# Kernel tuning notes

Hardware: AMD Instinct MI355X
Metric: run time of the kernel (lower is better)

Reference implementation:

```python
import jax, jax.numpy as jnp
import numpy as np

WS = (4, 4, 4)          # window size (s, h, w)
NUM_HEADS = 6
DIM = 192               # kv channels C
CS = 2                  # channel_scale; q/out channels = DIM // CS
B = 256                 # num_windows * batch


def _rel_pos_index(ws):
    """Reproduces the module's relative_position_index buffer (shape [8shw, 2shw])."""
    s, h, w = ws
    cs = np.repeat(np.arange(s), 2)
    ch = np.repeat(np.arange(h), 2)
    cw = np.repeat(np.arange(w), 2)
    coords = np.stack(np.meshgrid(cs, ch, cw, indexing='ij'))   # (3, 2s, 2h, 2w)
    cf = coords.reshape(3, -1)                                   # (3, T), T = 8shw
    rel = cf[:, :, None] - cf[:, None, :]                        # (3, T, T)
    rel = rel[:, :, ::4]                                         # (3, T, T//4)
    rel = np.ascontiguousarray(rel.transpose(1, 2, 0))           # (T, T//4, 3)
    rel[:, :, 0] += s - 1
    rel[:, :, 1] += h - 1
    rel[:, :, 2] += w - 1
    rel[:, :, 0] *= 3 * h - 1
    rel[:, :, 1] *= 2 * h - 1
    return rel.sum(-1).astype(np.int32)                          # (T, T//4)


def setup_inputs() -> dict:
    key = jax.random.key(0)
    ks = jax.random.split(key, 9)
    s, h, w = WS
    qN = 8 * s * h * w          # 512 query tokens per window
    N = qN // 4                 # 128 key/value tokens per window
    C = DIM
    qC = DIM // CS
    table_len = (4 * s - 1) * (4 * h - 1) * (4 * w - 1)
    return {
        'kv': jax.random.normal(ks[0], (B, N, C), jnp.float32),
        'q': jax.random.normal(ks[1], (B, qN, qC), jnp.float32),
        'w_kv': jax.random.normal(ks[2], (C, 2 * C), jnp.float32) * 0.02,
        'b_kv': jnp.zeros((2 * C,), jnp.float32),
        'w_q': jax.random.normal(ks[3], (qC, C), jnp.float32) * 0.02,
        'b_q': jnp.zeros((C,), jnp.float32),
        'w_proj': jax.random.normal(ks[4], (C, qC), jnp.float32) * 0.02,
        'b_proj': jnp.zeros((qC,), jnp.float32),
        'bias_table': jax.random.normal(ks[5], (table_len, NUM_HEADS), jnp.float32) * 0.02,
        'rel_index': jnp.asarray(_rel_pos_index(WS)),
    }


def reference(kv, q, w_kv, b_kv, w_q, b_q, w_proj, b_proj, bias_table, rel_index):
    B_, N, C = kv.shape
    d = C // NUM_HEADS
    scale = d ** -0.5
    # project kv -> k, v : (B_, nH, N, d)
    kvp = (kv @ w_kv + b_kv).reshape(B_, N, 2, NUM_HEADS, d)
    k = kvp[:, :, 0].transpose(0, 2, 1, 3)
    v = kvp[:, :, 1].transpose(0, 2, 1, 3)
    # project q : (B_, nH, qN, d), pre-scaled
    qp = (q @ w_q + b_q).reshape(B_, -1, NUM_HEADS, d).transpose(0, 2, 1, 3) * scale
    attn = jnp.einsum('bhqd,bhkd->bhqk', qp, k)          # (B_, nH, qN, N)
    bias = bias_table[rel_index]                          # (qN, N, nH) gather
    attn = attn + bias.transpose(2, 0, 1)[None]           # + (1, nH, qN, N)
    attn = jax.nn.softmax(attn, axis=-1)
    out = jnp.einsum('bhqk,bhkd->bhqd', attn, v)          # (B_, nH, qN, d)
    out = out.transpose(0, 2, 1, 3).reshape(B_, -1, C)    # (B_, qN, C)
    return out @ w_proj + b_proj                          # (B_, qN, C//CS)
```

## Files before the change

### kernel.cpp

```cpp
#include <hip/hip_runtime.h>
#include <hip/hip_bf16.h>

#define B_    256
#define NKV   128
#define NQ    512
#define CDIM  192
#define QCDIM 96
#define NH    6
#define DH    32
#define SCALE 0.17677669529663687f
#define LOG2E 1.4426950408889634f

typedef __hip_bfloat16 bf16;
typedef __attribute__((ext_vector_type(8))) short s16x8;
typedef __attribute__((ext_vector_type(4))) short s16x4;
typedef __attribute__((ext_vector_type(4))) float f32x4;
#define MFMA16(a, b, c) __builtin_amdgcn_mfma_f32_16x16x32_bf16(a, b, c, 0, 0, 0)

__device__ __forceinline__ float b2f(short s) {
    return __uint_as_float(((unsigned)(unsigned short)s) << 16);
}

#define OFF_BIASF 0
#define OFF_WKVF  786432
#define OFF_WQF   933888
#define OFF_WPF   970752
#define OFF_KF    1007616
#define OFF_VF    13590528

__global__ __launch_bounds__(256)
void precomp_all(const float* __restrict__ w_kv, const float* __restrict__ w_q,
                 const float* __restrict__ w_proj, const float* __restrict__ bias_table,
                 const int* __restrict__ rel_index,
                 bf16* __restrict__ biasF, bf16* __restrict__ wkvF,
                 bf16* __restrict__ wqF, bf16* __restrict__ wpF)
{
    const int i = blockIdx.x * 256 + threadIdx.x;
    if (i < 98304) {
        const int lane = i & 63, tl = (i >> 6) & 7, rowblk = (i >> 9) & 31, h = i >> 14;
        const int quad = lane >> 4, l16 = lane & 15;
        const int kvi = tl * 16 + l16;
        __align__(8) bf16 vr[4];
        #pragma unroll
        for (int r = 0; r < 4; ++r) {
            const int qrow = rowblk * 16 + quad * 4 + r;
            vr[r] = __float2bfloat16(bias_table[rel_index[qrow * NKV + kvi] * NH + h] * LOG2E);
        }
        *(uint2*)&biasF[i * 4] = *(uint2*)vr;
    } else if (i < 98304 + 73728) {
        const int i1 = i - 98304;
        const int j = i1 & 7, lane = (i1 >> 3) & 63, kk = (i1 >> 9) % 6, nt = i1 / 3072;
        const int quad = lane >> 4, l16 = lane & 15;
        wkvF[i1] = __float2bfloat16(w_kv[(kk * 32 + quad * 8 + j) * (2 * CDIM) + nt * 16 + l16]);
    } else if (i < 98304 + 92160) {
        const int i2 = i - 98304 - 73728;
        const int j = i2 & 7, lane = (i2 >> 3) & 63, kk = (i2 >> 9) % 3,
                  tl = (i2 / 1536) & 1, h = i2 / 3072;
        const int quad = lane >> 4, l16 = lane & 15;
        wqF[i2] = __float2bfloat16(w_q[(kk * 32 + quad * 8 + j) * CDIM + h * DH + tl * 16 + l16]
                                   * (SCALE * LOG2E));
    } else {
        const int i3 = i - 98304 - 92160;
        const int j = i3 & 7, lane = (i3 >> 3) & 63, tn = (i3 >> 9) % 6, h = i3 / 3072;
        const int quad = lane >> 4, l16 = lane & 15;
        wpF[i3] = __float2bfloat16(w_proj[(h * DH + quad * 8 + j) * QCDIM + tn * 16 + l16]);
    }
}

__global__ __launch_bounds__(512, 4)
void proj_kv(const float* __restrict__ kv, const float* __restrict__ b_kv,
             const bf16* __restrict__ wkvF, bf16* __restrict__ KF, bf16* __restrict__ VF)
{
    __shared__ __align__(16) char smem[52224];
    bf16* sA = (bf16*)smem;
    const int b = blockIdx.x, half = blockIdx.y, t = threadIdx.x;
    const int w = t >> 6, lane = t & 63, quad = lane >> 4, l16 = lane & 15;
    const f32x4 ZV = {0.f, 0.f, 0.f, 0.f};

    for (int f = t; f < 6144; f += 512) {
        const int r = f / 48, c4 = f % 48;
        const float4 v = *(const float4*)&kv[((size_t)b * NKV + r) * CDIM + c4 * 4];
        __align__(8) bf16 tmp[4] = {__float2bfloat16(v.x), __float2bfloat16(v.y),
                                    __float2bfloat16(v.z), __float2bfloat16(v.w)};
        *(uint2*)&sA[r * 200 + c4 * 4] = *(uint2*)tmp;
    }
    __syncthreads();

    f32x4 acc[12];
    #pragma unroll
    for (int i = 0; i < 12; ++i) acc[i] = ZV;
    for (int kk = 0; kk < 6; ++kk) {
        const s16x8 a = *(const s16x8*)&sA[(w * 16 + l16) * 200 + kk * 32 + quad * 8];
        #pragma unroll
        for (int nt = 0; nt < 12; ++nt) {
            const s16x8 bb = *(const s16x8*)&wkvF[(((half * 12 + nt) * 6 + kk) * 64 + lane) * 8];
            acc[nt] = MFMA16(a, bb, acc[nt]);
        }
    }
    __syncthreads();

    if (half == 0) {
        bf16* bufK = (bf16*)smem;
        #pragma unroll
        for (int nt = 0; nt < 12; ++nt) {
            const int col = nt * 16 + l16;
            const float bias = b_kv[col];
            #pragma unroll
            for (int r = 0; r < 4; ++r)
                bufK[(w * 16 + quad * 4 + r) * 200 + col] = __float2bfloat16(acc[nt][r] + bias);
        }
        __syncthreads();
        bf16* KF_b = KF + (size_t)b * 24576;
        #pragma unroll
        for (int i = 0; i < 6; ++i) {
            const int fr = w * 6 + i, h = fr >> 3, tl = fr & 7;
            const s16x8 v = *(const s16x8*)&bufK[(tl * 16 + l16) * 200 + h * DH + quad * 8];
            *(s16x8*)&KF_b[(size_t)(fr * 64 + lane) * 8] = v;
        }
    } else {
        bf16* bufV = (bf16*)smem;
        #pragma unroll
        for (int nt = 0; nt < 12; ++nt) {
            const int d = nt * 16 + l16;
            const float bias = b_kv[CDIM + d];
            __align__(8) bf16 tmp[4];
            #pragma unroll
            for (int r = 0; r < 4; ++r) tmp[r] = __float2bfloat16(acc[nt][r] + bias);
            *(uint2*)&bufV[d * 136 + w * 16 + quad * 4] = *(uint2*)tmp;
        }
        __syncthreads();
        bf16* VF_b = VF + (size_t)b * 24576;
        #pragma unroll
        for (int i = 0; i < 6; ++i) {
            const int fr = w * 6 + i, h = fr >> 3, tl = (fr >> 2) & 1, kk = fr & 3;
            const s16x8 v = *(const s16x8*)&bufV[(h * DH + tl * 16 + l16) * 136 + kk * 32 + quad * 8];
            *(s16x8*)&VF_b[(size_t)(fr * 64 + lane) * 8] = v;
        }
    }
}

__global__ __launch_bounds__(256, 4)
void attn_fused(const float* __restrict__ q, const float* __restrict__ b_q,
                const float* __restrict__ b_proj, const char* __restrict__ wsro,
                float* __restrict__ out)
{
    __shared__ __align__(16) bf16 sP[4 * 16 * 136];
    const int b = blockIdx.x, y = blockIdx.y;
    const int t = threadIdx.x;
    const int w = t >> 6, lane = t & 63, quad = lane >> 4, l16 = lane & 15;

    const bf16* biasF = (const bf16*)(wsro + OFF_BIASF);
    const bf16* wqF   = (const bf16*)(wsro + OFF_WQF);
    const bf16* wpF   = (const bf16*)(wsro + OFF_WPF);
    const bf16* KF_b  = (const bf16*)(wsro + OFF_KF) + (size_t)b * 24576;
    const bf16* VF_b  = (const bf16*)(wsro + OFF_VF) + (size_t)b * 24576;

    const int rb = y * 4 + w;
    bf16* myP = sP + w * 2176;

    s16x8 qa[3];
    #pragma unroll
    for (int kk = 0; kk < 3; ++kk) {
        const float* src = &q[((size_t)b * NQ + rb * 16 + l16) * QCDIM + kk * 32 + quad * 8];
        const float4 a0 = *(const float4*)src;
        const float4 a1 = *(const float4*)(src + 4);
        __align__(16) bf16 tmp[8] = {
            __float2bfloat16(a0.x), __float2bfloat16(a0.y), __float2bfloat16(a0.z),
            __float2bfloat16(a0.w), __float2bfloat16(a1.x), __float2bfloat16(a1.y),
            __float2bfloat16(a1.z), __float2bfloat16(a1.w)};
        qa[kk] = *(s16x8*)tmp;
    }

    f32x4 outacc[6];
    #pragma unroll
    for (int tn = 0; tn < 6; ++tn) {
        const float bp = b_proj[tn * 16 + l16];
        outacc[tn] = (f32x4){bp, bp, bp, bp};
    }

    for (int h = 0; h < NH; ++h) {
        s16x8 kf[8];
        #pragma unroll
        for (int t4 = 0; t4 < 8; ++t4)
            kf[t4] = *(const s16x8*)&KF_b[(size_t)((h * 8 + t4) * 64 + lane) * 8];
        s16x4 bb[8];
        #pragma unroll
        for (int t4 = 0; t4 < 8; ++t4)
            bb[t4] = *(const s16x4*)&biasF[(((h * 32 + rb) * 8 + t4) * 64 + lane) * 4];
        s16x8 wqf[6];
        #pragma unroll
        for (int i = 0; i < 6; ++i)
            wqf[i] = *(const s16x8*)&wqF[((h * 6 + i) * 64 + lane) * 8];

        f32x4 qacc[2];
        #pragma unroll
        for (int tl = 0; tl < 2; ++tl) {
            const float bq = b_q[h * DH + tl * 16 + l16] * (SCALE * LOG2E);
            qacc[tl] = (f32x4){bq, bq, bq, bq};
        }
        #pragma unroll
        for (int kk = 0; kk < 3; ++kk)
            #pragma unroll
            for (int tl = 0; tl < 2; ++tl)
                qacc[tl] = MFMA16(qa[kk], wqf[tl * 3 + kk], qacc[tl]);
        #pragma unroll
        for (int tl = 0; tl < 2; ++tl)
            #pragma unroll
            for (int r = 0; r < 4; ++r)
                myP[(quad * 4 + r) * 136 + tl * 16 + l16] = __float2bfloat16(qacc[tl][r]);

        s16x8 vf[8];
        #pragma unroll
        for (int i = 0; i < 8; ++i)
            vf[i] = *(const s16x8*)&VF_b[(size_t)((h * 8 + i) * 64 + lane) * 8];

        const s16x8 aQ = *(const s16x8*)&myP[l16 * 136 + quad * 8];

        f32x4 sacc[8];
        #pragma unroll
        for (int t4 = 0; t4 < 8; ++t4)
            #pragma unroll
            for (int r = 0; r < 4; ++r)
                sacc[t4][r] = b2f(bb[t4][r]);
        #pragma unroll
        for (int t4 = 0; t4 < 8; ++t4)
            sacc[t4] = MFMA16(aQ, kf[t4], sacc[t4]);
        float rs[4] = {0.f, 0.f, 0.f, 0.f};
        #pragma unroll
        for (int t4 = 0; t4 < 8; ++t4)
            #pragma unroll
            for (int r = 0; r < 4; ++r) {
                const float vv = __builtin_amdgcn_exp2f(sacc[t4][r]);
                rs[r] += vv;
                myP[(quad * 4 + r) * 136 + t4 * 16 + l16] = __float2bfloat16(vv);
            }

        s16x8 wpf[6];
        #pragma unroll
        for (int i = 0; i < 6; ++i)
            wpf[i] = *(const s16x8*)&wpF[((h * 6 + i) * 64 + lane) * 8];

        float inv[4];
        #pragma unroll
        for (int r = 0; r < 4; ++r) {
            float s = rs[r];
            #pragma unroll
            for (int off = 1; off < 16; off <<= 1) s += __shfl_xor(s, off, 16);
            inv[r] = 1.f / s;
        }

        f32x4 oacc[2];
        oacc[0] = (f32x4){0.f, 0.f, 0.f, 0.f};
        oacc[1] = (f32x4){0.f, 0.f, 0.f, 0.f};
        #pragma unroll
        for (int kk = 0; kk < 4; ++kk) {
            const s16x8 aP = *(const s16x8*)&myP[l16 * 136 + kk * 32 + quad * 8];
            #pragma unroll
            for (int tl = 0; tl < 2; ++tl)
                oacc[tl] = MFMA16(aP, vf[tl * 4 + kk], oacc[tl]);
        }
        #pragma unroll
        for (int tl = 0; tl < 2; ++tl)
            #pragma unroll
            for (int r = 0; r < 4; ++r)
                myP[(quad * 4 + r) * 136 + tl * 16 + l16] = __float2bfloat16(oacc[tl][r] * inv[r]);

        const s16x8 aO = *(const s16x8*)&myP[l16 * 136 + quad * 8];
        #pragma unroll
        for (int tn = 0; tn < 6; ++tn)
            outacc[tn] = MFMA16(aO, wpf[tn], outacc[tn]);
    }

    #pragma unroll
    for (int tn = 0; tn < 6; ++tn)
        #pragma unroll
        for (int r = 0; r < 4; ++r)
            out[((size_t)b * NQ + rb * 16 + quad * 4 + r) * QCDIM + tn * 16 + l16]
                = outacc[tn][r];
}

extern "C" void kernel_launch(void* const* d_in, const int* in_sizes, int n_in,
                              void* d_out, int out_size, void* d_ws, size_t ws_size,
                              hipStream_t stream)
{
    const float* kv       = (const float*)d_in[0];
    const float* q        = (const float*)d_in[1];
    const float* w_kv     = (const float*)d_in[2];
    const float* b_kv     = (const float*)d_in[3];
    const float* w_q      = (const float*)d_in[4];
    const float* b_q      = (const float*)d_in[5];
    const float* w_proj   = (const float*)d_in[6];
    const float* b_proj   = (const float*)d_in[7];
    const float* bias_tab = (const float*)d_in[8];
    const int*   rel_idx  = (const int*)d_in[9];
    char* ws = (char*)d_ws;

    precomp_all<<<816, 256, 0, stream>>>(w_kv, w_q, w_proj, bias_tab, rel_idx,
                                         (bf16*)(ws + OFF_BIASF), (bf16*)(ws + OFF_WKVF),
                                         (bf16*)(ws + OFF_WQF), (bf16*)(ws + OFF_WPF));
    proj_kv<<<dim3(B_, 2), 512, 0, stream>>>(kv, b_kv, (const bf16*)(ws + OFF_WKVF),
                                             (bf16*)(ws + OFF_KF), (bf16*)(ws + OFF_VF));
    attn_fused<<<dim3(B_, 8), 256, 0, stream>>>(q, b_q, b_proj, (const char*)ws,
                                                (float*)d_out);
}
```

Before: 210.8 us.

## Split proj_kv over token halves and double-buffer weight fragment loads

The KV projection kernel now launches twice as many blocks of 256 threads, each covering 64 of the 128 kv tokens, with LDS buffers shrunk to match. The K/V fragment write-out indexing is remapped for the half-token tiles. Weight B-fragments are software-pipelined in register double buffers so global loads overlap the MFMAs, and the bias values are hoisted into registers before the main loop. This aims for more blocks and better latency hiding in a small kernel, at the cost of higher register pressure and each block re-reading the full weight slice.

```diff
diff --git a/kernel.cpp b/kernel.cpp
--- a/kernel.cpp
+++ b/kernel.cpp
@@ -67,35 +67,54 @@
     }
 }
 
-__global__ __launch_bounds__(512, 4)
+__global__ __launch_bounds__(256, 3)
 void proj_kv(const float* __restrict__ kv, const float* __restrict__ b_kv,
              const bf16* __restrict__ wkvF, bf16* __restrict__ KF, bf16* __restrict__ VF)
 {
-    __shared__ __align__(16) char smem[52224];
+    __shared__ __align__(16) char smem[27648];
     bf16* sA = (bf16*)smem;
-    const int b = blockIdx.x, half = blockIdx.y, t = threadIdx.x;
+    const int b = blockIdx.x, half = blockIdx.y, half2 = blockIdx.z, t = threadIdx.x;
     const int w = t >> 6, lane = t & 63, quad = lane >> 4, l16 = lane & 15;
     const f32x4 ZV = {0.f, 0.f, 0.f, 0.f};
 
-    for (int f = t; f < 6144; f += 512) {
+    for (int f = t; f < 3072; f += 256) {
         const int r = f / 48, c4 = f % 48;
-        const float4 v = *(const float4*)&kv[((size_t)b * NKV + r) * CDIM + c4 * 4];
+        const float4 v = *(const float4*)&kv[((size_t)b * NKV + half2 * 64 + r) * CDIM + c4 * 4];
         __align__(8) bf16 tmp[4] = {__float2bfloat16(v.x), __float2bfloat16(v.y),
                                     __float2bfloat16(v.z), __float2bfloat16(v.w)};
         *(uint2*)&sA[r * 200 + c4 * 4] = *(uint2*)tmp;
     }
+
+    float bias[12];
+    #pragma unroll
+    for (int nt = 0; nt < 12; ++nt) bias[nt] = b_kv[half * CDIM + nt * 16 + l16];
+
     __syncthreads();
 
     f32x4 acc[12];
     #pragma unroll
     for (int i = 0; i < 12; ++i) acc[i] = ZV;
-    for (int kk = 0; kk < 6; ++kk) {
-        const s16x8 a = *(const s16x8*)&sA[(w * 16 + l16) * 200 + kk * 32 + quad * 8];
-        #pragma unroll
-        for (int nt = 0; nt < 12; ++nt) {
-            const s16x8 bb = *(const s16x8*)&wkvF[(((half * 12 + nt) * 6 + kk) * 64 + lane) * 8];
-            acc[nt] = MFMA16(a, bb, acc[nt]);
-        }
+
+    s16x8 fA[12], fB[12];
+    #pragma unroll
+    for (int nt = 0; nt < 12; ++nt)
+        fA[nt] = *(const s16x8*)&wkvF[(((half * 12 + nt) * 6 + 0) * 64 + lane) * 8];
+    #pragma unroll
+    for (int kk = 0; kk < 6; kk += 2) {
+        #pragma unroll
+        for (int nt = 0; nt < 12; ++nt)
+            fB[nt] = *(const s16x8*)&wkvF[(((half * 12 + nt) * 6 + kk + 1) * 64 + lane) * 8];
+        const s16x8 a0 = *(const s16x8*)&sA[(w * 16 + l16) * 200 + kk * 32 + quad * 8];
+        #pragma unroll
+        for (int nt = 0; nt < 12; ++nt) acc[nt] = MFMA16(a0, fA[nt], acc[nt]);
+        if (kk + 2 < 6) {
+            #pragma unroll
+            for (int nt = 0; nt < 12; ++nt)
+                fA[nt] = *(const s16x8*)&wkvF[(((half * 12 + nt) * 6 + kk + 2) * 64 + lane) * 8];
+        }
+        const s16x8 a1 = *(const s16x8*)&sA[(w * 16 + l16) * 200 + (kk + 1) * 32 + quad * 8];
+        #pragma unroll
+        for (int nt = 0; nt < 12; ++nt) acc[nt] = MFMA16(a1, fB[nt], acc[nt]);
     }
     __syncthreads();
 
@@ -104,37 +123,38 @@
         #pragma unroll
         for (int nt = 0; nt < 12; ++nt) {
             const int col = nt * 16 + l16;
-            const float bias = b_kv[col];
             #pragma unroll
             for (int r = 0; r < 4; ++r)
-                bufK[(w * 16 + quad * 4 + r) * 200 + col] = __float2bfloat16(acc[nt][r] + bias);
+                bufK[(w * 16 + quad * 4 + r) * 200 + col] = __float2bfloat16(acc[nt][r] + bias[nt]);
         }
         __syncthreads();
         bf16* KF_b = KF + (size_t)b * 24576;
         #pragma unroll
         for (int i = 0; i < 6; ++i) {
-            const int fr = w * 6 + i, h = fr >> 3, tl = fr & 7;
-            const s16x8 v = *(const s16x8*)&bufK[(tl * 16 + l16) * 200 + h * DH + quad * 8];
-            *(s16x8*)&KF_b[(size_t)(fr * 64 + lane) * 8] = v;
+            const int fl = w * 6 + i;
+            const int h = fl >> 2, tll = fl & 3, tl = half2 * 4 + tll;
+            const s16x8 v = *(const s16x8*)&bufK[(tll * 16 + l16) * 200 + h * DH + quad * 8];
+            *(s16x8*)&KF_b[(size_t)((h * 8 + tl) * 64 + lane) * 8] = v;
         }
     } else {
         bf16* bufV = (bf16*)smem;
         #pragma unroll
         for (int nt = 0; nt < 12; ++nt) {
             const int d = nt * 16 + l16;
-            const float bias = b_kv[CDIM + d];
             __align__(8) bf16 tmp[4];
             #pragma unroll
-            for (int r = 0; r < 4; ++r) tmp[r] = __float2bfloat16(acc[nt][r] + bias);
-            *(uint2*)&bufV[d * 136 + w * 16 + quad * 4] = *(uint2*)tmp;
+            for (int r = 0; r < 4; ++r) tmp[r] = __float2bfloat16(acc[nt][r] + bias[nt]);
+            *(uint2*)&bufV[d * 72 + w * 16 + quad * 4] = *(uint2*)tmp;
         }
         __syncthreads();
         bf16* VF_b = VF + (size_t)b * 24576;
         #pragma unroll
         for (int i = 0; i < 6; ++i) {
-            const int fr = w * 6 + i, h = fr >> 3, tl = (fr >> 2) & 1, kk = fr & 3;
-            const s16x8 v = *(const s16x8*)&bufV[(h * DH + tl * 16 + l16) * 136 + kk * 32 + quad * 8];
-            *(s16x8*)&VF_b[(size_t)(fr * 64 + lane) * 8] = v;
+            const int fl = w * 6 + i;
+            const int h = fl >> 2, rest = fl & 3, tl = rest >> 1, kkl = rest & 1;
+            const int kk = half2 * 2 + kkl;
+            const s16x8 v = *(const s16x8*)&bufV[(h * DH + tl * 16 + l16) * 72 + kkl * 32 + quad * 8];
+            *(s16x8*)&VF_b[(size_t)(((h * 2 + tl) * 4 + kk) * 64 + lane) * 8] = v;
         }
     }
 }
@@ -298,8 +318,8 @@
     precomp_all<<<816, 256, 0, stream>>>(w_kv, w_q, w_proj, bias_tab, rel_idx,
                                          (bf16*)(ws + OFF_BIASF), (bf16*)(ws + OFF_WKVF),
                                          (bf16*)(ws + OFF_WQF), (bf16*)(ws + OFF_WPF));
-    proj_kv<<<dim3(B_, 2), 512, 0, stream>>>(kv, b_kv, (const bf16*)(ws + OFF_WKVF),
-                                             (bf16*)(ws + OFF_KF), (bf16*)(ws + OFF_VF));
+    proj_kv<<<dim3(B_, 2, 2), 256, 0, stream>>>(kv, b_kv, (const bf16*)(ws + OFF_WKVF),
+                                                (bf16*)(ws + OFF_KF), (bf16*)(ws + OFF_VF));
     attn_fused<<<dim3(B_, 8), 256, 0, stream>>>(q, b_q, b_proj, (const char*)ws,
                                                 (float*)d_out);
 }
```

Result: no change. 214.2 us, median of 2 (+1.6%).
